# Optimization experiments

Measured on AMD Instinct MI355X. Metric: run time of the kernel, lower is better.

## Reference

```python
import jax, jax.numpy as jnp
import numpy as np

N, E, G = 2048, 65536, 32
F_ATOM, LAT, IN, ED, NB, L = 16, 64, 128, 32, 5, 5


def setup_inputs() -> dict:
    key = jax.random.key(0)
    ks = iter(jax.random.split(key, 64))
    nxt = lambda: next(ks)
    def w(shape):
        fan_in = shape[-2] if len(shape) >= 2 else 1
        return jax.random.normal(nxt(), shape, jnp.float32) / np.sqrt(fan_in)
    inp = {}
    inp['x'] = jax.random.normal(nxt(), (N, F_ATOM), jnp.float32)
    inp['t'] = jax.random.uniform(nxt(), (G, 1), jnp.float32)
    inp['z'] = jax.random.normal(nxt(), (N, LAT), jnp.float32)
    inp['edge_index'] = jax.random.randint(nxt(), (2, E), 0, N, jnp.int32)
    inp['edge_attr'] = jax.random.normal(nxt(), (E, NB), jnp.float32)
    inp['batch'] = jnp.sort(jax.random.randint(nxt(), (N,), 0, G, jnp.int32))
    inp['batch_edge_global'] = jax.random.randint(nxt(), (E,), 0, G, jnp.int32)
    # top-level dense layers
    inp['Wt_a'] = w((1, IN)); inp['bt_a'] = jnp.zeros((IN,))
    inp['Wt_b'] = w((1, ED)); inp['bt_b'] = jnp.zeros((ED,))
    inp['W_atom'] = w((F_ATOM, IN)); inp['b_atom'] = jnp.zeros((IN,))
    inp['W_bond'] = w((NB, ED)); inp['b_bond'] = jnp.zeros((ED,))
    inp['W_lat'] = w((LAT, IN)); inp['b_lat'] = jnp.zeros((IN,))
    inp['W_at'] = w((IN, IN)); inp['b_at'] = jnp.zeros((IN,))
    inp['W_bt'] = w((ED, ED)); inp['b_bt'] = jnp.zeros((ED,))
    # TopoEdgeGNN: L layers of edge-conditioned message passing with edge update
    inp['Wmsg'] = w((L, 2 * IN + ED, IN)); inp['bmsg'] = jnp.zeros((L, IN))
    inp['Wnode'] = w((L, 2 * IN, IN)); inp['bnode'] = jnp.zeros((L, IN))
    inp['Wedge'] = w((L, 2 * IN + ED, ED)); inp['bedge'] = jnp.zeros((L, ED))
    # prediction head
    inp['Wsh'] = w((IN, IN)); inp['bsh'] = jnp.zeros((IN,))
    inp['Wbm'] = w((ED, IN)); inp['bbm'] = jnp.zeros((IN,))
    inp['Wbl'] = w((IN, NB)); inp['bbl'] = jnp.zeros((NB,))
    inp['Wal'] = w((IN, F_ATOM + LAT)); inp['bal'] = jnp.zeros((F_ATOM + LAT,))
    return inp


def reference(x, t, z, edge_index, edge_attr, batch, batch_edge_global,
              Wt_a, bt_a, Wt_b, bt_b, W_atom, b_atom, W_bond, b_bond,
              W_lat, b_lat, W_at, b_at, W_bt, b_bt,
              Wmsg, bmsg, Wnode, bnode, Wedge, bedge,
              Wsh, bsh, Wbm, bbm, Wbl, bbl, Wal, bal):
    j, i = edge_index[0], edge_index[1]
    # time embeddings, gathered to nodes / edges
    ta = t @ Wt_a + bt_a            # [G, IN]
    tb = t @ Wt_b + bt_b            # [G, ED]
    tnode = ta[batch]               # [N, IN]
    tedge = tb[batch_edge_global]   # [E, ED]
    # node features
    s = x @ W_atom + b_atom
    s = (s + tnode) @ W_at + b_at
    s = s + (z @ W_lat + b_lat)
    # edge features
    e = edge_attr @ W_bond + b_bond
    e = (e + tedge) @ W_bt + b_bt
    # TopoEdgeGNN: message passing with residual node/edge updates
    for l in range(L):
        m = jax.nn.silu(jnp.concatenate([s[i], s[j], e], -1) @ Wmsg[l] + bmsg[l])  # [E, IN]
        agg = jax.ops.segment_sum(m, i, num_segments=N)                            # [N, IN]
        s = s + jax.nn.silu(jnp.concatenate([s, agg], -1) @ Wnode[l] + bnode[l])
        e = e + jax.nn.silu(jnp.concatenate([s[i], s[j], e], -1) @ Wedge[l] + bedge[l])
    # prediction head
    s2 = jax.nn.silu(s @ Wsh + bsh)
    al = s2 @ Wal + bal
    atoms_pred, latent_pred = al[:, :F_ATOM], al[:, F_ATOM:]
    # dense edge symmetrization: scatter edges into [N, N, ED], symmetrize, gather back
    e_dense = jnp.zeros((N, N, ED), e.dtype).at[j, i].set(e)
    e_dense = 0.5 * (e_dense + e_dense.transpose(1, 0, 2))
    e_sym = e_dense[j, i]           # [E, ED]
    f = jax.nn.silu(s2[i] + s2[j] + (e_sym @ Wbm + bbm))
    bonds_pred = f @ Wbl + bbl
    return latent_pred, atoms_pred, bonds_pred
```

## Files before the change

kernel.cpp:

```cpp
#include <hip/hip_runtime.h>
#include <hip/hip_bf16.h>

#define NN 2048
#define NE 65536
#define NG 32
#define CIN 128
#define CED 32
#define CLAT 64
#define CFA 16
#define CNB 5
#define NL 5

#define OFF_AT (NN * CLAT)
#define OFF_B  (NN * CLAT + NN * CFA)

typedef __attribute__((ext_vector_type(8))) short bf16x8;
typedef __attribute__((ext_vector_type(4))) float f32x4;

__device__ __forceinline__ float silu_f(float v) { return v / (1.0f + __expf(-v)); }
__device__ __forceinline__ short f2bs(float v) {
    __hip_bfloat16 h = __float2bfloat16(v);
    return *reinterpret_cast<short*>(&h);
}
__device__ __forceinline__ unsigned pack2(float a, float b) {
    return ((unsigned)(unsigned short)f2bs(b) << 16) | (unsigned short)f2bs(a);
}

__global__ void k_pack_w(const float* __restrict__ Wmsg, const float* __restrict__ Wedge,
                         const float* __restrict__ Wnode, const float* __restrict__ Wsh,
                         const float* __restrict__ Wal, const float* __restrict__ Wbm,
                         short* __restrict__ Wpn, short* __restrict__ Wpsh,
                         short* __restrict__ Wpal, short* __restrict__ Wpbm,
                         short* __restrict__ Wproj, short* __restrict__ W3m, short* __restrict__ We3)
{
    int idx = blockIdx.x * 256 + threadIdx.x;
    int j = idx & 7, t0 = idx >> 3, lane = t0 & 63, t = t0 >> 6;
    int kq = (lane >> 4) * 8 + j, n16 = lane & 15;
    if (idx < NL * 8 * 8 * 64 * 8) {
        int nt = t & 7, kt = (t >> 3) & 7, l = t >> 6;
        Wpn[idx] = f2bs(Wnode[((size_t)l * 256 + kt * 32 + kq) * CIN + nt * 16 + n16]);
    }
    if (idx < 4 * 8 * 64 * 8) {
        int nt = t & 7, kt = t >> 3;
        Wpsh[idx] = f2bs(Wsh[(size_t)(kt * 32 + kq) * CIN + nt * 16 + n16]);
    }
    if (idx < 4 * 5 * 64 * 8) {
        int nt = t % 5, kt = t / 5;
        Wpal[idx] = f2bs(Wal[(size_t)(kt * 32 + kq) * 80 + nt * 16 + n16]);
    }
    if (idx < 8 * 64 * 8) {
        int nt = t & 7;
        Wpbm[idx] = f2bs(Wbm[(size_t)kq * CIN + nt * 16 + n16]);
    }
    if (idx < 6 * 4 * 20 * 64 * 8) {
        int nt = t % 20; int t2 = t / 20; int kt = t2 & 3; int slot = t2 >> 2;
        int k = kt * 32 + kq;
        float v;
        if (nt < 16) {
            int msgl = slot % 5;
            int srcK = (nt < 8) ? k : 128 + k;
            int col = (nt & 7) * 16 + n16;
            v = Wmsg[((size_t)msgl * 288 + srcK) * CIN + col];
        } else {
            int edgel = (slot == 0) ? 0 : slot - 1;
            int srcK = (nt < 18) ? k : 128 + k;
            int col = (nt & 1) * 16 + n16;
            v = Wedge[((size_t)edgel * 288 + srcK) * CED + col];
        }
        Wproj[idx] = f2bs(v);
    }
    if (idx < NL * 8 * 64 * 8) {
        int nt = t & 7, l = t >> 3;
        W3m[idx] = f2bs(Wmsg[((size_t)l * 288 + 256 + kq) * CIN + nt * 16 + n16]);
    }
    if (idx < NL * 2 * 64 * 8) {
        int nt = t & 1, l = t >> 1;
        We3[idx] = f2bs(Wedge[((size_t)l * 288 + 256 + kq) * CED + nt * 16 + n16]);
    }
}

__global__ __launch_bounds__(128) void k_init_s(
    const float* __restrict__ x, const float* __restrict__ t,
    const float* __restrict__ z, const int* __restrict__ batch,
    const float* __restrict__ Wt_a, const float* __restrict__ bt_a,
    const float* __restrict__ W_atom, const float* __restrict__ b_atom,
    const float* __restrict__ W_lat, const float* __restrict__ b_lat,
    const float* __restrict__ W_at, const float* __restrict__ b_at,
    float* __restrict__ s, short* __restrict__ s_bf)
{
    const int NB = 16;
    int nb0 = blockIdx.x * NB, c = threadIdx.x;
    __shared__ float xs[NB * CFA];
    __shared__ float zs[NB * CLAT];
    __shared__ float tmp[NB * CIN];
    __shared__ float tv[NB];
    if (c < NB * CFA / 4) ((float4*)xs)[c] = ((const float4*)x)[nb0 * (CFA / 4) + c];
    for (int q = c; q < NB * CLAT / 4; q += 128) ((float4*)zs)[q] = ((const float4*)z)[nb0 * (CLAT / 4) + q];
    if (c < NB) tv[c] = t[batch[nb0 + c]];
    __syncthreads();
    float wta = Wt_a[c], base0 = b_atom[c] + bt_a[c];
    float acc[NB];
#pragma unroll
    for (int nd = 0; nd < NB; nd++) acc[nd] = base0 + tv[nd] * wta;
    for (int k = 0; k < CFA; k++) {
        float w = W_atom[k * CIN + c];
#pragma unroll
        for (int nd = 0; nd < NB; nd++) acc[nd] += xs[nd * CFA + k] * w;
    }
#pragma unroll
    for (int nd = 0; nd < NB; nd++) tmp[nd * CIN + c] = acc[nd];
    __syncthreads();
    float base1 = b_at[c] + b_lat[c];
    float acc2[NB];
#pragma unroll
    for (int nd = 0; nd < NB; nd++) acc2[nd] = base1;
    for (int k4 = 0; k4 < CIN / 4; k4++) {
        float w0 = W_at[(4 * k4 + 0) * CIN + c], w1 = W_at[(4 * k4 + 1) * CIN + c];
        float w2 = W_at[(4 * k4 + 2) * CIN + c], w3 = W_at[(4 * k4 + 3) * CIN + c];
#pragma unroll
        for (int nd = 0; nd < NB; nd++) {
            float4 f = *(const float4*)&tmp[nd * CIN + 4 * k4];
            acc2[nd] += f.x * w0 + f.y * w1 + f.z * w2 + f.w * w3;
        }
    }
    for (int k4 = 0; k4 < CLAT / 4; k4++) {
        float w0 = W_lat[(4 * k4 + 0) * CIN + c], w1 = W_lat[(4 * k4 + 1) * CIN + c];
        float w2 = W_lat[(4 * k4 + 2) * CIN + c], w3 = W_lat[(4 * k4 + 3) * CIN + c];
#pragma unroll
        for (int nd = 0; nd < NB; nd++) {
            float4 f = *(const float4*)&zs[nd * CLAT + 4 * k4];
            acc2[nd] += f.x * w0 + f.y * w1 + f.z * w2 + f.w * w3;
        }
    }
#pragma unroll
    for (int nd = 0; nd < NB; nd++) {
        s[(nb0 + nd) * CIN + c] = acc2[nd];
        s_bf[(nb0 + nd) * CIN + c] = f2bs(acc2[nd]);
    }
}

__global__ void k_init_e(const float* __restrict__ ea, const float* __restrict__ t,
                         const int* __restrict__ beg, const int* __restrict__ jj, const int* __restrict__ ii,
                         const float* __restrict__ Wt_b, const float* __restrict__ bt_b,
                         const float* __restrict__ W_bond, const float* __restrict__ b_bond,
                         const float* __restrict__ W_bt, const float* __restrict__ b_bt,
                         float* __restrict__ e, short* __restrict__ e_bf, int* __restrict__ map,
                         int* __restrict__ cnt)
{
    int le = threadIdx.x >> 5, c = threadIdx.x & 31;
    int k = blockIdx.x * 8 + le;
    __shared__ float tmp[8][CED];
    float tg = t[beg[k]];
    float acc = b_bond[c] + tg * Wt_b[c] + bt_b[c];
#pragma unroll
    for (int b = 0; b < CNB; b++) acc += ea[k * CNB + b] * W_bond[b * CED + c];
    tmp[le][c] = acc;
    __syncthreads();
    float acc2 = b_bt[c];
#pragma unroll
    for (int d = 0; d < CED; d++) acc2 += tmp[le][d] * W_bt[d * CED + c];
    e[k * CED + c] = acc2;
    e_bf[k * CED + c] = f2bs(acc2);
    if (c == 0) {
        atomicMax(&map[jj[k] * NN + ii[k]], k);
        atomicAdd(&cnt[ii[k]], 1);
    }
}

__global__ __launch_bounds__(256) void k_prefix(const int* __restrict__ cnt, int* __restrict__ rowpos)
{
    __shared__ int part[256];
    int tid = threadIdx.x;
    int loc[8], sum = 0;
#pragma unroll
    for (int q = 0; q < 8; q++) { loc[q] = cnt[tid * 8 + q]; sum += loc[q]; }
    part[tid] = sum;
    __syncthreads();
    if (tid == 0) {
        int r = 0;
        for (int i = 0; i < 256; i++) { int v = part[i]; part[i] = r; r += v; }
    }
    __syncthreads();
    int r = part[tid];
#pragma unroll
    for (int q = 0; q < 8; q++) { rowpos[tid * 8 + q] = r; r += loc[q]; }
}

__global__ void k_perm(const int* __restrict__ ii, int* __restrict__ rowpos, int* __restrict__ perm)
{
    int k = blockIdx.x * 256 + threadIdx.x;
    if (k < NE) {
        int p = atomicAdd(&rowpos[ii[k]], 1);
        perm[p] = k;
    }
}

template<bool DO_NODE>
__global__ __launch_bounds__(256) void k_node_proj(
    float* __restrict__ s, short* __restrict__ s_bf, float* __restrict__ agg,
    const short* __restrict__ Wpn_l, const float* __restrict__ bnode_l,
    const short* __restrict__ Wproj, float* __restrict__ U, float* __restrict__ V,
    float* __restrict__ P, float* __restrict__ Q)
{
    __shared__ short feat[16 * 264];
    __shared__ short feat2[16 * 136];
    int tid = threadIdx.x;
    int nb0 = blockIdx.x * 16;
    int lane = tid & 63, w = tid >> 6;
    int quad = lane >> 4, n16 = lane & 15;

    if (DO_NODE) {
        {
            int kl = tid >> 4, c = tid & 15;
            *(uint4*)&feat[kl * 264 + c * 8] = ((const uint4*)s_bf)[(size_t)(nb0 + kl) * 16 + c];
        }
        for (int idx = tid; idx < 16 * 32; idx += 256) {
            int kl = idx >> 5, c = idx & 31;
            size_t gix = (size_t)(nb0 + kl) * 32 + c;
            float4 v = ((const float4*)agg)[gix];
            ((float4*)agg)[gix] = (float4){0.f, 0.f, 0.f, 0.f};
            uint2 p; p.x = pack2(v.x, v.y); p.y = pack2(v.z, v.w);
            *(uint2*)&feat[kl * 264 + 128 + 4 * c] = p;
        }
        __syncthreads();
        f32x4 acc[2];
        acc[0] = (f32x4){0.f, 0.f, 0.f, 0.f};
        acc[1] = (f32x4){0.f, 0.f, 0.f, 0.f};
        const short* fbase = feat + n16 * 264 + quad * 8;
#pragma unroll
        for (int kt = 0; kt < 8; kt++) {
            bf16x8 a = *(const bf16x8*)(fbase + kt * 32);
#pragma unroll
            for (int n2 = 0; n2 < 2; n2++) {
                int nt = w * 2 + n2;
                bf16x8 b = *(const bf16x8*)(Wpn_l + ((size_t)(kt * 8 + nt) * 64 + lane) * 8);
                acc[n2] = __builtin_amdgcn_mfma_f32_16x16x32_bf16(a, b, acc[n2], 0, 0, 0);
            }
        }
#pragma unroll
        for (int n2 = 0; n2 < 2; n2++) {
            int col = (w * 2 + n2) * 16 + n16;
            float bb = bnode_l[col];
#pragma unroll
            for (int r = 0; r < 4; r++) {
                int row = quad * 4 + r;
                size_t ix = (size_t)(nb0 + row) * CIN + col;
                float v = s[ix] + silu_f(acc[n2][r] + bb);
                s[ix] = v;
                short bv = f2bs(v);
                s_bf[ix] = bv;
                feat2[row * 136 + col] = bv;
            }
        }
        __syncthreads();
    } else {
        int kl = tid >> 4, c = tid & 15;
        *(uint4*)&feat2[kl * 136 + c * 8] = ((const uint4*)s_bf)[(size_t)(nb0 + kl) * 16 + c];
        __syncthreads();
    }

    f32x4 accp[5];
#pragma unroll
    for (int t2 = 0; t2 < 5; t2++) accp[t2] = (f32x4){0.f, 0.f, 0.f, 0.f};
    const short* abase = feat2 + n16 * 136 + quad * 8;
#pragma unroll
    for (int kt = 0; kt < 4; kt++) {
        bf16x8 a = *(const bf16x8*)(abase + kt * 32);
#pragma unroll
        for (int n5 = 0; n5 < 5; n5++) {
            int nt = w * 5 + n5;
            bf16x8 b = *(const bf16x8*)(Wproj + ((size_t)(kt * 20 + nt) * 64 + lane) * 8);
            accp[n5] = __builtin_amdgcn_mfma_f32_16x16x32_bf16(a, b, accp[n5], 0, 0, 0);
        }
    }
#pragma unroll
    for (int n5 = 0; n5 < 5; n5++) {
        int nt = w * 5 + n5;
#pragma unroll
        for (int r = 0; r < 4; r++) {
            int node = nb0 + quad * 4 + r;
            float v = accp[n5][r];
            if (nt < 8)       U[(size_t)node * CIN + nt * 16 + n16] = v;
            else if (nt < 16) V[(size_t)node * CIN + (nt - 8) * 16 + n16] = v;
            else if (nt < 18) P[(size_t)node * CED + (nt - 16) * 16 + n16] = v;
            else              Q[(size_t)node * CED + (nt - 18) * 16 + n16] = v;
        }
    }
}

template<bool DO_EDGE, bool DO_MSG>
__global__ __launch_bounds__(256) void k_em(
    const short* __restrict__ e_bf_in,
    const int* __restrict__ ii, const int* __restrict__ jj, const int* __restrict__ perm,
    const short* __restrict__ We3p, const float* __restrict__ bedge,
    const float* __restrict__ P, const float* __restrict__ Q,
    float* __restrict__ e, short* __restrict__ e_bf,
    const short* __restrict__ W3mp, const float* __restrict__ bmsg,
    const float* __restrict__ U, const float* __restrict__ V,
    float* __restrict__ agg)
{
    __shared__ short feat_e[64 * 40];
    __shared__ float uv[64 * 132];
    __shared__ float pq[64 * 36];
    __shared__ int sii[64], sjj[64], sek[64];
    int tid = threadIdx.x;
    int e0 = blockIdx.x * 64;
    if (tid < 64) {
        int k = perm[e0 + tid];
        sek[tid] = k;
        sii[tid] = ii[k];
        sjj[tid] = jj[k];
    }
    __syncthreads();
    {
        int kl = tid >> 2, c = tid & 3;
        uint4 v = ((const uint4*)e_bf_in)[(size_t)sek[kl] * 4 + c];
        *(uint4*)&feat_e[kl * 40 + c * 8] = v;
    }
    if (DO_EDGE) {
        for (int idx = tid; idx < 64 * 8; idx += 256) {
            int kl = idx >> 3, c = idx & 7;
            float4 a = ((const float4*)P)[(size_t)sii[kl] * 8 + c];
            float4 b = ((const float4*)Q)[(size_t)sjj[kl] * 8 + c];
            *(float4*)&pq[kl * 36 + 4 * c] = (float4){a.x + b.x, a.y + b.y, a.z + b.z, a.w + b.w};
        }
    }
    if (DO_MSG) {
        for (int idx = tid; idx < 64 * 32; idx += 256) {
            int kl = idx >> 5, c = idx & 31;
            float4 a = ((const float4*)U)[(size_t)sii[kl] * 32 + c];
            float4 b = ((const float4*)V)[(size_t)sjj[kl] * 32 + c];
            *(float4*)&uv[kl * 132 + 4 * c] = (float4){a.x + b.x, a.y + b.y, a.z + b.z, a.w + b.w};
        }
    }
    __syncthreads();
    int lane = tid & 63, w = tid >> 6;
    int quad = lane >> 4, n16 = lane & 15;
    const short* abase = feat_e + (w * 16 + n16) * 40 + quad * 8;
    bf16x8 a = *(const bf16x8*)abase;

    if (DO_EDGE) {
        f32x4 acc_e[2];
        acc_e[0] = (f32x4){0.f, 0.f, 0.f, 0.f};
        acc_e[1] = (f32x4){0.f, 0.f, 0.f, 0.f};
#pragma unroll
        for (int nt = 0; nt < 2; nt++) {
            bf16x8 b = *(const bf16x8*)(We3p + ((size_t)(nt * 64 + lane)) * 8);
            acc_e[nt] = __builtin_amdgcn_mfma_f32_16x16x32_bf16(a, b, acc_e[nt], 0, 0, 0);
        }
#pragma unroll
        for (int nt = 0; nt < 2; nt++) {
            int ch = nt * 16 + n16;
            float bb = bedge[ch];
#pragma unroll
            for (int r = 0; r < 4; r++) {
                int el = w * 16 + quad * 4 + r;
                size_t ix = (size_t)sek[el] * CED + ch;
                float v = e[ix] + silu_f(acc_e[nt][r] + bb + pq[el * 36 + ch]);
                e[ix] = v;
                short bv = f2bs(v);
                e_bf[ix] = bv;
                feat_e[el * 40 + ch] = bv;
            }
        }
        a = *(const bf16x8*)abase;
    }

    if (DO_MSG) {
        f32x4 acc_m[8];
#pragma unroll
        for (int t2 = 0; t2 < 8; t2++) acc_m[t2] = (f32x4){0.f, 0.f, 0.f, 0.f};
#pragma unroll
        for (int nt = 0; nt < 8; nt++) {
            bf16x8 b = *(const bf16x8*)(W3mp + ((size_t)(nt * 64 + lane)) * 8);
            acc_m[nt] = __builtin_amdgcn_mfma_f32_16x16x32_bf16(a, b, acc_m[nt], 0, 0, 0);
        }
#pragma unroll
        for (int nt = 0; nt < 8; nt++) {
            int ch = nt * 16 + n16;
            float bb = bmsg[ch];
#pragma unroll
            for (int r = 0; r < 4; r++) {
                int el = w * 16 + quad * 4 + r;
                int lix = el * 132 + ch;
                float m = silu_f(acc_m[nt][r] + bb + uv[lix]);
                uv[lix] = m;
            }
        }
        __syncthreads();
        if (tid < 128) {
            int c = tid;
            float run = 0.f;
            int cur = sii[0];
            for (int r = 0; r < 64; r++) {
                int tg = sii[r];
                if (tg != cur) { atomicAdd(&agg[(size_t)cur * CIN + c], run); run = 0.f; cur = tg; }
                run += uv[r * 132 + c];
            }
            atomicAdd(&agg[(size_t)cur * CIN + c], run);
        }
    }
}

__global__ __launch_bounds__(256) void k_post_node_mfma(
    const short* __restrict__ s_bf,
    const short* __restrict__ Wpsh, const float* __restrict__ bsh,
    const short* __restrict__ Wpal, const float* __restrict__ bal,
    float* __restrict__ s2, float* __restrict__ out)
{
    __shared__ short feat[16 * 136];
    __shared__ short feat_s2[16 * 136];
    int tid = threadIdx.x;
    int nb0 = blockIdx.x * 16;
    int lane = tid & 63, w = tid >> 6;
    int quad = lane >> 4, n16 = lane & 15;
    {
        int kl = tid >> 4, c = tid & 15;
        *(uint4*)&feat[kl * 136 + c * 8] = ((const uint4*)s_bf)[(size_t)(nb0 + kl) * 16 + c];
    }
    __syncthreads();
    const short* fbase = feat + n16 * 136 + quad * 8;
    f32x4 acc[2];
    acc[0] = (f32x4){0.f, 0.f, 0.f, 0.f};
    acc[1] = (f32x4){0.f, 0.f, 0.f, 0.f};
#pragma unroll
    for (int kt = 0; kt < 4; kt++) {
        bf16x8 a = *(const bf16x8*)(fbase + kt * 32);
#pragma unroll
        for (int n2 = 0; n2 < 2; n2++) {
            int nt = w * 2 + n2;
            bf16x8 b = *(const bf16x8*)(Wpsh + ((size_t)(kt * 8 + nt) * 64 + lane) * 8);
            acc[n2] = __builtin_amdgcn_mfma_f32_16x16x32_bf16(a, b, acc[n2], 0, 0, 0);
        }
    }
#pragma unroll
    for (int n2 = 0; n2 < 2; n2++) {
        int col = (w * 2 + n2) * 16 + n16;
        float bb = bsh[col];
#pragma unroll
        for (int r = 0; r < 4; r++) {
            int row = quad * 4 + r;
            float v = silu_f(acc[n2][r] + bb);
            s2[(size_t)(nb0 + row) * CIN + col] = v;
            feat_s2[row * 136 + col] = f2bs(v);
        }
    }
    __syncthreads();
    const short* abase = feat_s2 + n16 * 136 + quad * 8;
    f32x4 acca[2];
    acca[0] = (f32x4){0.f, 0.f, 0.f, 0.f};
    acca[1] = (f32x4){0.f, 0.f, 0.f, 0.f};
    int nAl = (w == 0) ? 2 : 1;
    int ntl[2] = {w, 4};
#pragma unroll
    for (int kt = 0; kt < 4; kt++) {
        bf16x8 a = *(const bf16x8*)(abase + kt * 32);
#pragma unroll
        for (int q = 0; q < 2; q++) {
            if (q < nAl) {
                bf16x8 b = *(const bf16x8*)(Wpal + ((size_t)(kt * 5 + ntl[q]) * 64 + lane) * 8);
                acca[q] = __builtin_amdgcn_mfma_f32_16x16x32_bf16(a, b, acca[q], 0, 0, 0);
            }
        }
    }
#pragma unroll
    for (int q = 0; q < 2; q++) {
        if (q < nAl) {
            int col = ntl[q] * 16 + n16;
            float bb = bal[col];
#pragma unroll
            for (int r = 0; r < 4; r++) {
                int node = nb0 + quad * 4 + r;
                float v = acca[q][r] + bb;
                if (col < CFA) out[OFF_AT + node * CFA + col] = v;
                else           out[(size_t)node * CLAT + (col - CFA)] = v;
            }
        }
    }
}

__global__ __launch_bounds__(256) void k_post_edge_mfma(
    const float* __restrict__ s2, const float* __restrict__ e,
    const int* __restrict__ ii, const int* __restrict__ jj, const int* __restrict__ map,
    const short* __restrict__ Wpbm, const float* __restrict__ bbm,
    const float* __restrict__ Wbl, const float* __restrict__ bbl,
    float* __restrict__ out)
{
    __shared__ int sii[64], sjj[64], skf[64], skb[64];
    __shared__ short esym[64 * 40];
    __shared__ float sbias[64 * 132];
    int tid = threadIdx.x;
    int e0 = blockIdx.x * 64;
    if (tid < 64) sii[tid] = ii[e0 + tid];
    else if (tid < 128) sjj[tid - 64] = jj[e0 + tid - 64];
    __syncthreads();
    if (tid < 64) skf[tid] = map[(size_t)sjj[tid] * NN + sii[tid]];
    else if (tid < 128) skb[tid - 64] = map[(size_t)sii[tid - 64] * NN + sjj[tid - 64]];
    __syncthreads();
    for (int idx = tid; idx < 64 * 8; idx += 256) {
        int kl = idx >> 3, c = idx & 7;
        float4 a = ((const float4*)e)[(size_t)skf[kl] * 8 + c];
        int kb = skb[kl];
        float4 b = {0.f, 0.f, 0.f, 0.f};
        if (kb >= 0) b = ((const float4*)e)[(size_t)kb * 8 + c];
        uint2 p; p.x = pack2(0.5f * (a.x + b.x), 0.5f * (a.y + b.y));
        p.y = pack2(0.5f * (a.z + b.z), 0.5f * (a.w + b.w));
        *(uint2*)&esym[kl * 40 + 4 * c] = p;
    }
    for (int idx = tid; idx < 64 * 32; idx += 256) {
        int kl = idx >> 5, c = idx & 31;
        float4 a = ((const float4*)s2)[(size_t)sii[kl] * 32 + c];
        float4 b = ((const float4*)s2)[(size_t)sjj[kl] * 32 + c];
        float4 v = {a.x + b.x, a.y + b.y, a.z + b.z, a.w + b.w};
        *(float4*)&sbias[kl * 132 + 4 * c] = v;
    }
    __syncthreads();
    int lane = tid & 63, w = tid >> 6;
    int quad = lane >> 4, n16 = lane & 15;
    bf16x8 a = *(const bf16x8*)(esym + (w * 16 + n16) * 40 + quad * 8);
    f32x4 acc[8];
#pragma unroll
    for (int nt = 0; nt < 8; nt++) {
        bf16x8 b = *(const bf16x8*)(Wpbm + ((size_t)nt * 64 + lane) * 8);
        f32x4 zero = {0.f, 0.f, 0.f, 0.f};
        acc[nt] = __builtin_amdgcn_mfma_f32_16x16x32_bf16(a, b, zero, 0, 0, 0);
    }
    float f[8][4];
#pragma unroll
    for (int nt = 0; nt < 8; nt++) {
        int col = nt * 16 + n16;
        float bb = bbm[col];
#pragma unroll
        for (int r = 0; r < 4; r++) {
            int row = w * 16 + quad * 4 + r;
            f[nt][r] = silu_f(acc[nt][r] + bb + sbias[row * 132 + col]);
        }
    }
    __syncthreads();
    float* fshT = sbias;
#pragma unroll
    for (int nt = 0; nt < 8; nt++) {
        int col = nt * 16 + n16;
#pragma unroll
        for (int r = 0; r < 4; r++) {
            int row = w * 16 + quad * 4 + r;
            fshT[col * 66 + row] = f[nt][r];
        }
    }
    __syncthreads();
    for (int idx = tid; idx < 64 * CNB; idx += 256) {
        int kl = idx / CNB, b = idx - kl * CNB;
        float acc3 = bbl[b];
        for (int d = 0; d < CIN; d++) acc3 += fshT[d * 66 + kl] * Wbl[d * CNB + b];
        out[OFF_B + (size_t)(e0 + kl) * CNB + b] = acc3;
    }
}

extern "C" void kernel_launch(void* const* d_in, const int* in_sizes, int n_in,
                              void* d_out, int out_size, void* d_ws, size_t ws_size,
                              hipStream_t stream) {
    const float* x      = (const float*)d_in[0];
    const float* t      = (const float*)d_in[1];
    const float* z      = (const float*)d_in[2];
    const int*   eidx   = (const int*)d_in[3];
    const int*   jj     = eidx;
    const int*   ii     = eidx + NE;
    const float* ea     = (const float*)d_in[4];
    const int*   batch  = (const int*)d_in[5];
    const int*   beg    = (const int*)d_in[6];
    const float* Wt_a   = (const float*)d_in[7];
    const float* bt_a   = (const float*)d_in[8];
    const float* Wt_b   = (const float*)d_in[9];
    const float* bt_b   = (const float*)d_in[10];
    const float* W_atom = (const float*)d_in[11];
    const float* b_atom = (const float*)d_in[12];
    const float* W_bond = (const float*)d_in[13];
    const float* b_bond = (const float*)d_in[14];
    const float* W_lat  = (const float*)d_in[15];
    const float* b_lat  = (const float*)d_in[16];
    const float* W_at   = (const float*)d_in[17];
    const float* b_at   = (const float*)d_in[18];
    const float* W_bt   = (const float*)d_in[19];
    const float* b_bt   = (const float*)d_in[20];
    const float* Wmsg   = (const float*)d_in[21];
    const float* bmsg   = (const float*)d_in[22];
    const float* Wnode  = (const float*)d_in[23];
    const float* bnode  = (const float*)d_in[24];
    const float* Wedge  = (const float*)d_in[25];
    const float* bedge  = (const float*)d_in[26];
    const float* Wsh    = (const float*)d_in[27];
    const float* bsh    = (const float*)d_in[28];
    const float* Wbm    = (const float*)d_in[29];
    const float* bbm    = (const float*)d_in[30];
    const float* Wbl    = (const float*)d_in[31];
    const float* bbl    = (const float*)d_in[32];
    const float* Wal    = (const float*)d_in[33];
    const float* bal    = (const float*)d_in[34];

    float* s      = (float*)d_ws;
    float* e      = s + (size_t)NN * CIN;
    float* agg    = e + (size_t)NE * CED;
    int*   cnt    = (int*)(agg + (size_t)NN * CIN);
    int*   rowpos = cnt + NN;
    int*   perm   = rowpos + NN;
    float* s2     = (float*)(perm + NE);
    float* U      = s2 + (size_t)NN * CIN;
    float* V      = U + (size_t)NN * CIN;
    float* P      = V + (size_t)NN * CIN;
    float* Q      = P + (size_t)NN * CED;
    int*   map    = (int*)(Q + (size_t)NN * CED);
    short* s_bf   = (short*)(map + (size_t)NN * NN);
    short* e_bf   = s_bf + (size_t)NN * CIN;
    short* Wpn    = e_bf + (size_t)NE * CED;
    short* Wpsh   = Wpn + (size_t)NL * 8 * 8 * 64 * 8;
    short* Wpal   = Wpsh + (size_t)4 * 8 * 64 * 8;
    short* Wpbm   = Wpal + (size_t)4 * 5 * 64 * 8;
    short* Wproj  = Wpbm + (size_t)8 * 64 * 8;
    short* W3m    = Wproj + (size_t)6 * 4 * 20 * 64 * 8;
    short* We3    = W3m + (size_t)NL * 8 * 64 * 8;
    float* out    = (float*)d_out;

    hipMemsetAsync(map, 0xFF, (size_t)NN * NN * sizeof(int), stream);
    hipMemsetAsync(agg, 0, ((size_t)NN * CIN + NN) * sizeof(float), stream);
    k_pack_w<<<960, 256, 0, stream>>>(Wmsg, Wedge, Wnode, Wsh, Wal, Wbm,
                                      Wpn, Wpsh, Wpal, Wpbm, Wproj, W3m, We3);
    k_init_s<<<NN / 16, 128, 0, stream>>>(x, t, z, batch, Wt_a, bt_a, W_atom, b_atom,
                                          W_lat, b_lat, W_at, b_at, s, s_bf);
    k_init_e<<<NE / 8, 256, 0, stream>>>(ea, t, beg, jj, ii, Wt_b, bt_b, W_bond, b_bond,
                                         W_bt, b_bt, e, e_bf, map, cnt);
    k_prefix<<<1, 256, 0, stream>>>(cnt, rowpos);
    k_perm<<<NE / 256, 256, 0, stream>>>(ii, rowpos, perm);

    k_node_proj<false><<<NN / 16, 256, 0, stream>>>(s, s_bf, agg, nullptr, nullptr,
                                                    Wproj, U, V, P, Q);
    k_em<false, true><<<NE / 64, 256, 0, stream>>>(e_bf, ii, jj, perm,
                                                   nullptr, nullptr, P, Q, e, e_bf,
                                                   W3m, bmsg, U, V, agg);
    for (int l = 0; l < NL; l++) {
        k_node_proj<true><<<NN / 16, 256, 0, stream>>>(s, s_bf, agg,
                                                       Wpn + (size_t)l * 8 * 8 * 64 * 8,
                                                       bnode + l * CIN,
                                                       Wproj + (size_t)(l + 1) * 4 * 20 * 64 * 8,
                                                       U, V, P, Q);
        if (l < NL - 1) {
            k_em<true, true><<<NE / 64, 256, 0, stream>>>(e_bf, ii, jj, perm,
                                                          We3 + (size_t)l * 2 * 64 * 8,
                                                          bedge + l * CED, P, Q, e, e_bf,
                                                          W3m + (size_t)(l + 1) * 8 * 64 * 8,
                                                          bmsg + (l + 1) * CIN, U, V, agg);
        } else {
            k_em<true, false><<<NE / 64, 256, 0, stream>>>(e_bf, ii, jj, perm,
                                                           We3 + (size_t)l * 2 * 64 * 8,
                                                           bedge + l * CED, P, Q, e, e_bf,
                                                           nullptr, nullptr, nullptr, nullptr, agg);
        }
    }
    k_post_node_mfma<<<NN / 16, 256, 0, stream>>>(s_bf, Wpsh, bsh, Wpal, bal, s2, out);
    k_post_edge_mfma<<<NE / 64, 256, 0, stream>>>(s2, e, ii, jj, map, Wpbm, bbm, Wbl, bbl, out);
}
```

Measured before the change: 397.8 us.

## Store edge features in destination-sorted order and merge prologue kernels

Edge features e and e_bf are now written in CSR order, sorted by destination node, through an inverse permutation. This lets the per-layer edge/message kernels read them contiguously instead of gathering through perm, and the sorted i/j index arrays are precomputed. The weight packing, node init and degree counting are merged into one prologue launch, and edge init now runs after the permutation using shared-memory weights and 64 edges per block. The post-edge kernel maps symmetric lookups through invp, which adds one extra indirection there.

Result: faster. 383.8 us (-3.5%).

```diff
diff --git a/kernel.cpp b/kernel.cpp
--- a/kernel.cpp
+++ b/kernel.cpp
@@ -26,144 +26,126 @@
     return ((unsigned)(unsigned short)f2bs(b) << 16) | (unsigned short)f2bs(a);
 }
 
-__global__ void k_pack_w(const float* __restrict__ Wmsg, const float* __restrict__ Wedge,
-                         const float* __restrict__ Wnode, const float* __restrict__ Wsh,
-                         const float* __restrict__ Wal, const float* __restrict__ Wbm,
-                         short* __restrict__ Wpn, short* __restrict__ Wpsh,
-                         short* __restrict__ Wpal, short* __restrict__ Wpbm,
-                         short* __restrict__ Wproj, short* __restrict__ W3m, short* __restrict__ We3)
-{
-    int idx = blockIdx.x * 256 + threadIdx.x;
-    int j = idx & 7, t0 = idx >> 3, lane = t0 & 63, t = t0 >> 6;
-    int kq = (lane >> 4) * 8 + j, n16 = lane & 15;
-    if (idx < NL * 8 * 8 * 64 * 8) {
-        int nt = t & 7, kt = (t >> 3) & 7, l = t >> 6;
-        Wpn[idx] = f2bs(Wnode[((size_t)l * 256 + kt * 32 + kq) * CIN + nt * 16 + n16]);
-    }
-    if (idx < 4 * 8 * 64 * 8) {
-        int nt = t & 7, kt = t >> 3;
-        Wpsh[idx] = f2bs(Wsh[(size_t)(kt * 32 + kq) * CIN + nt * 16 + n16]);
-    }
-    if (idx < 4 * 5 * 64 * 8) {
-        int nt = t % 5, kt = t / 5;
-        Wpal[idx] = f2bs(Wal[(size_t)(kt * 32 + kq) * 80 + nt * 16 + n16]);
-    }
-    if (idx < 8 * 64 * 8) {
-        int nt = t & 7;
-        Wpbm[idx] = f2bs(Wbm[(size_t)kq * CIN + nt * 16 + n16]);
-    }
-    if (idx < 6 * 4 * 20 * 64 * 8) {
-        int nt = t % 20; int t2 = t / 20; int kt = t2 & 3; int slot = t2 >> 2;
-        int k = kt * 32 + kq;
-        float v;
-        if (nt < 16) {
-            int msgl = slot % 5;
-            int srcK = (nt < 8) ? k : 128 + k;
-            int col = (nt & 7) * 16 + n16;
-            v = Wmsg[((size_t)msgl * 288 + srcK) * CIN + col];
-        } else {
-            int edgel = (slot == 0) ? 0 : slot - 1;
-            int srcK = (nt < 18) ? k : 128 + k;
-            int col = (nt & 1) * 16 + n16;
-            v = Wedge[((size_t)edgel * 288 + srcK) * CED + col];
-        }
-        Wproj[idx] = f2bs(v);
-    }
-    if (idx < NL * 8 * 64 * 8) {
-        int nt = t & 7, l = t >> 3;
-        W3m[idx] = f2bs(Wmsg[((size_t)l * 288 + 256 + kq) * CIN + nt * 16 + n16]);
-    }
-    if (idx < NL * 2 * 64 * 8) {
-        int nt = t & 1, l = t >> 1;
-        We3[idx] = f2bs(Wedge[((size_t)l * 288 + 256 + kq) * CED + nt * 16 + n16]);
-    }
-}
-
-__global__ __launch_bounds__(128) void k_init_s(
+__global__ __launch_bounds__(256) void k_prologue(
+    const float* __restrict__ Wmsg, const float* __restrict__ Wedge,
+    const float* __restrict__ Wnode, const float* __restrict__ Wsh,
+    const float* __restrict__ Wal, const float* __restrict__ Wbm,
+    short* __restrict__ Wpn, short* __restrict__ Wpsh,
+    short* __restrict__ Wpal, short* __restrict__ Wpbm,
+    short* __restrict__ Wproj, short* __restrict__ W3m, short* __restrict__ We3,
     const float* __restrict__ x, const float* __restrict__ t,
     const float* __restrict__ z, const int* __restrict__ batch,
     const float* __restrict__ Wt_a, const float* __restrict__ bt_a,
     const float* __restrict__ W_atom, const float* __restrict__ b_atom,
     const float* __restrict__ W_lat, const float* __restrict__ b_lat,
     const float* __restrict__ W_at, const float* __restrict__ b_at,
-    float* __restrict__ s, short* __restrict__ s_bf)
-{
-    const int NB = 16;
-    int nb0 = blockIdx.x * NB, c = threadIdx.x;
-    __shared__ float xs[NB * CFA];
-    __shared__ float zs[NB * CLAT];
-    __shared__ float tmp[NB * CIN];
-    __shared__ float tv[NB];
-    if (c < NB * CFA / 4) ((float4*)xs)[c] = ((const float4*)x)[nb0 * (CFA / 4) + c];
-    for (int q = c; q < NB * CLAT / 4; q += 128) ((float4*)zs)[q] = ((const float4*)z)[nb0 * (CLAT / 4) + q];
-    if (c < NB) tv[c] = t[batch[nb0 + c]];
-    __syncthreads();
-    float wta = Wt_a[c], base0 = b_atom[c] + bt_a[c];
-    float acc[NB];
-#pragma unroll
-    for (int nd = 0; nd < NB; nd++) acc[nd] = base0 + tv[nd] * wta;
-    for (int k = 0; k < CFA; k++) {
-        float w = W_atom[k * CIN + c];
-#pragma unroll
-        for (int nd = 0; nd < NB; nd++) acc[nd] += xs[nd * CFA + k] * w;
-    }
-#pragma unroll
-    for (int nd = 0; nd < NB; nd++) tmp[nd * CIN + c] = acc[nd];
-    __syncthreads();
-    float base1 = b_at[c] + b_lat[c];
-    float acc2[NB];
-#pragma unroll
-    for (int nd = 0; nd < NB; nd++) acc2[nd] = base1;
-    for (int k4 = 0; k4 < CIN / 4; k4++) {
-        float w0 = W_at[(4 * k4 + 0) * CIN + c], w1 = W_at[(4 * k4 + 1) * CIN + c];
-        float w2 = W_at[(4 * k4 + 2) * CIN + c], w3 = W_at[(4 * k4 + 3) * CIN + c];
-#pragma unroll
-        for (int nd = 0; nd < NB; nd++) {
-            float4 f = *(const float4*)&tmp[nd * CIN + 4 * k4];
-            acc2[nd] += f.x * w0 + f.y * w1 + f.z * w2 + f.w * w3;
-        }
-    }
-    for (int k4 = 0; k4 < CLAT / 4; k4++) {
-        float w0 = W_lat[(4 * k4 + 0) * CIN + c], w1 = W_lat[(4 * k4 + 1) * CIN + c];
-        float w2 = W_lat[(4 * k4 + 2) * CIN + c], w3 = W_lat[(4 * k4 + 3) * CIN + c];
-#pragma unroll
-        for (int nd = 0; nd < NB; nd++) {
-            float4 f = *(const float4*)&zs[nd * CLAT + 4 * k4];
-            acc2[nd] += f.x * w0 + f.y * w1 + f.z * w2 + f.w * w3;
-        }
-    }
-#pragma unroll
-    for (int nd = 0; nd < NB; nd++) {
-        s[(nb0 + nd) * CIN + c] = acc2[nd];
-        s_bf[(nb0 + nd) * CIN + c] = f2bs(acc2[nd]);
-    }
-}
-
-__global__ void k_init_e(const float* __restrict__ ea, const float* __restrict__ t,
-                         const int* __restrict__ beg, const int* __restrict__ jj, const int* __restrict__ ii,
-                         const float* __restrict__ Wt_b, const float* __restrict__ bt_b,
-                         const float* __restrict__ W_bond, const float* __restrict__ b_bond,
-                         const float* __restrict__ W_bt, const float* __restrict__ b_bt,
-                         float* __restrict__ e, short* __restrict__ e_bf, int* __restrict__ map,
-                         int* __restrict__ cnt)
-{
-    int le = threadIdx.x >> 5, c = threadIdx.x & 31;
-    int k = blockIdx.x * 8 + le;
-    __shared__ float tmp[8][CED];
-    float tg = t[beg[k]];
-    float acc = b_bond[c] + tg * Wt_b[c] + bt_b[c];
-#pragma unroll
-    for (int b = 0; b < CNB; b++) acc += ea[k * CNB + b] * W_bond[b * CED + c];
-    tmp[le][c] = acc;
-    __syncthreads();
-    float acc2 = b_bt[c];
-#pragma unroll
-    for (int d = 0; d < CED; d++) acc2 += tmp[le][d] * W_bt[d * CED + c];
-    e[k * CED + c] = acc2;
-    e_bf[k * CED + c] = f2bs(acc2);
-    if (c == 0) {
-        atomicMax(&map[jj[k] * NN + ii[k]], k);
-        atomicAdd(&cnt[ii[k]], 1);
+    float* __restrict__ s, short* __restrict__ s_bf,
+    const int* __restrict__ ii, int* __restrict__ cnt)
+{
+    int b = blockIdx.x, tid = threadIdx.x;
+    if (b < 960) {
+        int idx = b * 256 + tid;
+        int j = idx & 7, t0 = idx >> 3, lane = t0 & 63, tt = t0 >> 6;
+        int kq = (lane >> 4) * 8 + j, n16 = lane & 15;
+        if (idx < NL * 8 * 8 * 64 * 8) {
+            int nt = tt & 7, kt = (tt >> 3) & 7, l = tt >> 6;
+            Wpn[idx] = f2bs(Wnode[((size_t)l * 256 + kt * 32 + kq) * CIN + nt * 16 + n16]);
+        }
+        if (idx < 4 * 8 * 64 * 8) {
+            int nt = tt & 7, kt = tt >> 3;
+            Wpsh[idx] = f2bs(Wsh[(size_t)(kt * 32 + kq) * CIN + nt * 16 + n16]);
+        }
+        if (idx < 4 * 5 * 64 * 8) {
+            int nt = tt % 5, kt = tt / 5;
+            Wpal[idx] = f2bs(Wal[(size_t)(kt * 32 + kq) * 80 + nt * 16 + n16]);
+        }
+        if (idx < 8 * 64 * 8) {
+            int nt = tt & 7;
+            Wpbm[idx] = f2bs(Wbm[(size_t)kq * CIN + nt * 16 + n16]);
+        }
+        if (idx < 6 * 4 * 20 * 64 * 8) {
+            int nt = tt % 20; int t2 = tt / 20; int kt = t2 & 3; int slot = t2 >> 2;
+            int k = kt * 32 + kq;
+            float v;
+            if (nt < 16) {
+                int msgl = slot % 5;
+                int srcK = (nt < 8) ? k : 128 + k;
+                int col = (nt & 7) * 16 + n16;
+                v = Wmsg[((size_t)msgl * 288 + srcK) * CIN + col];
+            } else {
+                int edgel = (slot == 0) ? 0 : slot - 1;
+                int srcK = (nt < 18) ? k : 128 + k;
+                int col = (nt & 1) * 16 + n16;
+                v = Wedge[((size_t)edgel * 288 + srcK) * CED + col];
+            }
+            Wproj[idx] = f2bs(v);
+        }
+        if (idx < NL * 8 * 64 * 8) {
+            int nt = tt & 7, l = tt >> 3;
+            W3m[idx] = f2bs(Wmsg[((size_t)l * 288 + 256 + kq) * CIN + nt * 16 + n16]);
+        }
+        if (idx < NL * 2 * 64 * 8) {
+            int nt = tt & 1, l = tt >> 1;
+            We3[idx] = f2bs(Wedge[((size_t)l * 288 + 256 + kq) * CED + nt * 16 + n16]);
+        }
+    } else if (b < 1088) {
+        __shared__ float xs[16 * CFA];
+        __shared__ float zs[16 * CLAT];
+        __shared__ float tmp[16 * CIN];
+        __shared__ float tv[16];
+        int nb0 = (b - 960) * 16;
+        int c = tid & 127, h = tid >> 7;
+        if (tid < 16 * CFA / 4) ((float4*)xs)[tid] = ((const float4*)x)[nb0 * (CFA / 4) + tid];
+        if (tid < 16 * CLAT / 4) ((float4*)zs)[tid] = ((const float4*)z)[nb0 * (CLAT / 4) + tid];
+        if (tid < 16) tv[tid] = t[batch[nb0 + tid]];
+        __syncthreads();
+        float wta = Wt_a[c], base0 = b_atom[c] + bt_a[c];
+        float acc[8];
+#pragma unroll
+        for (int q = 0; q < 8; q++) acc[q] = base0 + tv[h * 8 + q] * wta;
+        for (int k = 0; k < CFA; k++) {
+            float w = W_atom[k * CIN + c];
+#pragma unroll
+            for (int q = 0; q < 8; q++) acc[q] += xs[(h * 8 + q) * CFA + k] * w;
+        }
+#pragma unroll
+        for (int q = 0; q < 8; q++) tmp[(h * 8 + q) * CIN + c] = acc[q];
+        __syncthreads();
+        float base1 = b_at[c] + b_lat[c];
+        float acc2[8];
+#pragma unroll
+        for (int q = 0; q < 8; q++) acc2[q] = base1;
+        for (int k4 = 0; k4 < CIN / 4; k4++) {
+            float w0 = W_at[(4 * k4 + 0) * CIN + c], w1 = W_at[(4 * k4 + 1) * CIN + c];
+            float w2 = W_at[(4 * k4 + 2) * CIN + c], w3 = W_at[(4 * k4 + 3) * CIN + c];
+#pragma unroll
+            for (int q = 0; q < 8; q++) {
+                float4 f = *(const float4*)&tmp[(h * 8 + q) * CIN + 4 * k4];
+                acc2[q] += f.x * w0 + f.y * w1 + f.z * w2 + f.w * w3;
+            }
+        }
+        for (int k4 = 0; k4 < CLAT / 4; k4++) {
+            float w0 = W_lat[(4 * k4 + 0) * CIN + c], w1 = W_lat[(4 * k4 + 1) * CIN + c];
+            float w2 = W_lat[(4 * k4 + 2) * CIN + c], w3 = W_lat[(4 * k4 + 3) * CIN + c];
+#pragma unroll
+            for (int q = 0; q < 8; q++) {
+                float4 f = *(const float4*)&zs[(h * 8 + q) * CLAT + 4 * k4];
+                acc2[q] += f.x * w0 + f.y * w1 + f.z * w2 + f.w * w3;
+            }
+        }
+#pragma unroll
+        for (int q = 0; q < 8; q++) {
+            int nd = nb0 + h * 8 + q;
+            s[(size_t)nd * CIN + c] = acc2[q];
+            s_bf[(size_t)nd * CIN + c] = f2bs(acc2[q]);
+        }
+    } else {
+        int base = (b - 1088) * 1024;
+#pragma unroll
+        for (int q = 0; q < 4; q++) {
+            int k = base + q * 256 + tid;
+            atomicAdd(&cnt[ii[k]], 1);
+        }
     }
 }
 
@@ -186,12 +168,64 @@
     for (int q = 0; q < 8; q++) { rowpos[tid * 8 + q] = r; r += loc[q]; }
 }
 
-__global__ void k_perm(const int* __restrict__ ii, int* __restrict__ rowpos, int* __restrict__ perm)
+__global__ void k_perm(const int* __restrict__ ii, const int* __restrict__ jj,
+                       int* __restrict__ rowpos, int* __restrict__ invp,
+                       int* __restrict__ i_s, int* __restrict__ j_s)
 {
     int k = blockIdx.x * 256 + threadIdx.x;
-    if (k < NE) {
-        int p = atomicAdd(&rowpos[ii[k]], 1);
-        perm[p] = k;
+    int iv = ii[k];
+    int p = atomicAdd(&rowpos[iv], 1);
+    invp[k] = p;
+    i_s[p] = iv;
+    j_s[p] = jj[k];
+}
+
+__global__ __launch_bounds__(256) void k_init_e(
+    const float* __restrict__ ea, const float* __restrict__ t,
+    const int* __restrict__ beg, const int* __restrict__ jj, const int* __restrict__ ii,
+    const int* __restrict__ invp,
+    const float* __restrict__ Wt_b, const float* __restrict__ bt_b,
+    const float* __restrict__ W_bond, const float* __restrict__ b_bond,
+    const float* __restrict__ W_bt, const float* __restrict__ b_bt,
+    float* __restrict__ e, short* __restrict__ e_bf, int* __restrict__ map)
+{
+    __shared__ float eas[64 * 5];
+    __shared__ float tv[64];
+    __shared__ int sp[64];
+    __shared__ float tmp[64][33];
+    __shared__ float wbt[32 * 32];
+    __shared__ float wbond[5 * 32];
+    __shared__ float cb[32], wtb[32], bbt2[32];
+    int tid = threadIdx.x;
+    int k0 = blockIdx.x * 64;
+    for (int idx = tid; idx < 320; idx += 256) eas[idx] = ea[(size_t)k0 * 5 + idx];
+    if (tid < 64) { tv[tid] = t[beg[k0 + tid]]; sp[tid] = invp[k0 + tid]; }
+    for (int idx = tid; idx < 1024; idx += 256) wbt[idx] = W_bt[idx];
+    if (tid < 160) wbond[tid] = W_bond[tid];
+    if (tid < 32) { cb[tid] = b_bond[tid] + bt_b[tid]; wtb[tid] = Wt_b[tid]; bbt2[tid] = b_bt[tid]; }
+    __syncthreads();
+    int ch = tid & 31, eg = tid >> 5;
+#pragma unroll
+    for (int q = 0; q < 8; q++) {
+        int le = eg * 8 + q;
+        float acc = cb[ch] + tv[le] * wtb[ch];
+#pragma unroll
+        for (int bb = 0; bb < CNB; bb++) acc += eas[le * 5 + bb] * wbond[bb * 32 + ch];
+        tmp[le][ch] = acc;
+    }
+    __syncthreads();
+#pragma unroll
+    for (int q = 0; q < 8; q++) {
+        int le = eg * 8 + q;
+        float acc2 = bbt2[ch];
+        for (int d = 0; d < 32; d++) acc2 += tmp[le][d] * wbt[d * 32 + ch];
+        size_t ix = (size_t)sp[le] * CED + ch;
+        e[ix] = acc2;
+        e_bf[ix] = f2bs(acc2);
+        if (ch == 0) {
+            int k = k0 + le;
+            atomicMax(&map[(size_t)jj[k] * NN + ii[k]], k);
+        }
     }
 }
 
@@ -291,7 +325,7 @@
 template<bool DO_EDGE, bool DO_MSG>
 __global__ __launch_bounds__(256) void k_em(
     const short* __restrict__ e_bf_in,
-    const int* __restrict__ ii, const int* __restrict__ jj, const int* __restrict__ perm,
+    const int* __restrict__ i_s, const int* __restrict__ j_s,
     const short* __restrict__ We3p, const float* __restrict__ bedge,
     const float* __restrict__ P, const float* __restrict__ Q,
     float* __restrict__ e, short* __restrict__ e_bf,
@@ -302,19 +336,15 @@
     __shared__ short feat_e[64 * 40];
     __shared__ float uv[64 * 132];
     __shared__ float pq[64 * 36];
-    __shared__ int sii[64], sjj[64], sek[64];
+    __shared__ int sii[64], sjj[64];
     int tid = threadIdx.x;
     int e0 = blockIdx.x * 64;
-    if (tid < 64) {
-        int k = perm[e0 + tid];
-        sek[tid] = k;
-        sii[tid] = ii[k];
-        sjj[tid] = jj[k];
-    }
+    if (tid < 64) sii[tid] = i_s[e0 + tid];
+    else if (tid < 128) sjj[tid - 64] = j_s[e0 + tid - 64];
     __syncthreads();
     {
         int kl = tid >> 2, c = tid & 3;
-        uint4 v = ((const uint4*)e_bf_in)[(size_t)sek[kl] * 4 + c];
+        uint4 v = ((const uint4*)e_bf_in)[(size_t)e0 * 4 + tid];
         *(uint4*)&feat_e[kl * 40 + c * 8] = v;
     }
     if (DO_EDGE) {
@@ -355,7 +385,7 @@
 #pragma unroll
             for (int r = 0; r < 4; r++) {
                 int el = w * 16 + quad * 4 + r;
-                size_t ix = (size_t)sek[el] * CED + ch;
+                size_t ix = (size_t)(e0 + el) * CED + ch;
                 float v = e[ix] + silu_f(acc_e[nt][r] + bb + pq[el * 36 + ch]);
                 e[ix] = v;
                 short bv = f2bs(v);
@@ -481,7 +511,8 @@
 
 __global__ __launch_bounds__(256) void k_post_edge_mfma(
     const float* __restrict__ s2, const float* __restrict__ e,
-    const int* __restrict__ ii, const int* __restrict__ jj, const int* __restrict__ map,
+    const int* __restrict__ ii, const int* __restrict__ jj,
+    const int* __restrict__ map, const int* __restrict__ invp,
     const short* __restrict__ Wpbm, const float* __restrict__ bbm,
     const float* __restrict__ Wbl, const float* __restrict__ bbl,
     float* __restrict__ out)
@@ -494,8 +525,11 @@
     if (tid < 64) sii[tid] = ii[e0 + tid];
     else if (tid < 128) sjj[tid - 64] = jj[e0 + tid - 64];
     __syncthreads();
-    if (tid < 64) skf[tid] = map[(size_t)sjj[tid] * NN + sii[tid]];
-    else if (tid < 128) skb[tid - 64] = map[(size_t)sii[tid - 64] * NN + sjj[tid - 64]];
+    if (tid < 64) skf[tid] = invp[map[(size_t)sjj[tid] * NN + sii[tid]]];
+    else if (tid < 128) {
+        int m = map[(size_t)sii[tid - 64] * NN + sjj[tid - 64]];
+        skb[tid - 64] = (m >= 0) ? invp[m] : -1;
+    }
     __syncthreads();
     for (int idx = tid; idx < 64 * 8; idx += 256) {
         int kl = idx >> 3, c = idx & 7;
@@ -602,8 +636,10 @@
     float* agg    = e + (size_t)NE * CED;
     int*   cnt    = (int*)(agg + (size_t)NN * CIN);
     int*   rowpos = cnt + NN;
-    int*   perm   = rowpos + NN;
-    float* s2     = (float*)(perm + NE);
+    int*   invp   = rowpos + NN;
+    int*   i_s    = invp + NE;
+    int*   j_s    = i_s + NE;
+    float* s2     = (float*)(j_s + NE);
     float* U      = s2 + (size_t)NN * CIN;
     float* V      = U + (size_t)NN * CIN;
     float* P      = V + (size_t)NN * CIN;
@@ -622,18 +658,18 @@
 
     hipMemsetAsync(map, 0xFF, (size_t)NN * NN * sizeof(int), stream);
     hipMemsetAsync(agg, 0, ((size_t)NN * CIN + NN) * sizeof(float), stream);
-    k_pack_w<<<960, 256, 0, stream>>>(Wmsg, Wedge, Wnode, Wsh, Wal, Wbm,
-                                      Wpn, Wpsh, Wpal, Wpbm, Wproj, W3m, We3);
-    k_init_s<<<NN / 16, 128, 0, stream>>>(x, t, z, batch, Wt_a, bt_a, W_atom, b_atom,
-                                          W_lat, b_lat, W_at, b_at, s, s_bf);
-    k_init_e<<<NE / 8, 256, 0, stream>>>(ea, t, beg, jj, ii, Wt_b, bt_b, W_bond, b_bond,
-                                         W_bt, b_bt, e, e_bf, map, cnt);
+    k_prologue<<<1152, 256, 0, stream>>>(Wmsg, Wedge, Wnode, Wsh, Wal, Wbm,
+                                         Wpn, Wpsh, Wpal, Wpbm, Wproj, W3m, We3,
+                                         x, t, z, batch, Wt_a, bt_a, W_atom, b_atom,
+                                         W_lat, b_lat, W_at, b_at, s, s_bf, ii, cnt);
     k_prefix<<<1, 256, 0, stream>>>(cnt, rowpos);
-    k_perm<<<NE / 256, 256, 0, stream>>>(ii, rowpos, perm);
+    k_perm<<<NE / 256, 256, 0, stream>>>(ii, jj, rowpos, invp, i_s, j_s);
+    k_init_e<<<NE / 64, 256, 0, stream>>>(ea, t, beg, jj, ii, invp, Wt_b, bt_b,
+                                          W_bond, b_bond, W_bt, b_bt, e, e_bf, map);
 
     k_node_proj<false><<<NN / 16, 256, 0, stream>>>(s, s_bf, agg, nullptr, nullptr,
                                                     Wproj, U, V, P, Q);
-    k_em<false, true><<<NE / 64, 256, 0, stream>>>(e_bf, ii, jj, perm,
+    k_em<false, true><<<NE / 64, 256, 0, stream>>>(e_bf, i_s, j_s,
                                                    nullptr, nullptr, P, Q, e, e_bf,
                                                    W3m, bmsg, U, V, agg);
     for (int l = 0; l < NL; l++) {
@@ -643,18 +679,19 @@
                                                        Wproj + (size_t)(l + 1) * 4 * 20 * 64 * 8,
                                                        U, V, P, Q);
         if (l < NL - 1) {
-            k_em<true, true><<<NE / 64, 256, 0, stream>>>(e_bf, ii, jj, perm,
+            k_em<true, true><<<NE / 64, 256, 0, stream>>>(e_bf, i_s, j_s,
                                                           We3 + (size_t)l * 2 * 64 * 8,
                                                           bedge + l * CED, P, Q, e, e_bf,
                                                           W3m + (size_t)(l + 1) * 8 * 64 * 8,
                                                           bmsg + (l + 1) * CIN, U, V, agg);
         } else {
-            k_em<true, false><<<NE / 64, 256, 0, stream>>>(e_bf, ii, jj, perm,
+            k_em<true, false><<<NE / 64, 256, 0, stream>>>(e_bf, i_s, j_s,
                                                            We3 + (size_t)l * 2 * 64 * 8,
                                                            bedge + l * CED, P, Q, e, e_bf,
                                                            nullptr, nullptr, nullptr, nullptr, agg);
         }
     }
     k_post_node_mfma<<<NN / 16, 256, 0, stream>>>(s_bf, Wpsh, bsh, Wpal, bal, s2, out);
-    k_post_edge_mfma<<<NE / 64, 256, 0, stream>>>(s2, e, ii, jj, map, Wpbm, bbm, Wbl, bbl, out);
-}
+    k_post_edge_mfma<<<NE / 64, 256, 0, stream>>>(s2, e, ii, jj, map, invp,
+                                                  Wpbm, bbm, Wbl, bbl, out);
+}
```
